# Kernel optimization log

Measured on AMD Instinct MI355X. Metric: run time of the kernel, lower is better.

## Reference

```python
import jax, jax.numpy as jnp
import numpy as np

N_NODES = 50000
N_EDGES = 800000
HIDDEN = 128
NUM_LAYERS = 3
NEG_SLOPE = 0.2  # PyG GATConv default leaky_relu slope


def setup_inputs() -> dict:
    key = jax.random.key(0)
    ks = jax.random.split(key, 10)
    d = HIDDEN
    glorot = 1.0 / np.sqrt(d)
    inp = {
        "x": jax.random.normal(ks[0], (N_NODES, d), dtype=jnp.float32),
        "edge_index": jax.random.randint(ks[1], (2, N_EDGES), 0, N_NODES, dtype=jnp.int32),
        "edge_mask": jax.random.uniform(ks[2], (N_EDGES,), dtype=jnp.float32),
        # GATConv params (heads=1)
        "W_gat": jax.random.normal(ks[3], (d, d), dtype=jnp.float32) * glorot,
        "a_src": jax.random.normal(ks[4], (d,), dtype=jnp.float32) * glorot,
        "a_dst": jax.random.normal(ks[5], (d,), dtype=jnp.float32) * glorot,
        "b_gat": jnp.zeros((d,), dtype=jnp.float32),
        # Stacked GCNConv params
        "W_gcn": jax.random.normal(ks[6], (NUM_LAYERS, d, d), dtype=jnp.float32) * glorot,
        "b_gcn": jnp.zeros((NUM_LAYERS, d), dtype=jnp.float32),
    }
    return inp


def _seg_softmax(e, seg, n):
    m = jax.ops.segment_max(e, seg, num_segments=n)
    p = jnp.exp(e - m[seg])
    s = jax.ops.segment_sum(p, seg, num_segments=n)
    return p / s[seg]


def reference(x, edge_index, edge_mask, W_gat, a_src, a_dst, b_gat, W_gcn, b_gcn):
    N = x.shape[0]
    loops = jnp.arange(N, dtype=edge_index.dtype)
    src = jnp.concatenate([edge_index[0], loops])  # [E+N] with self loops
    dst = jnp.concatenate([edge_index[1], loops])

    # --- GATConv (heads=1, add_self_loops=True); edge_attr ignored (edge_dim=None) ---
    xp = x @ W_gat                                      # [N, d]
    e = jax.nn.leaky_relu((xp @ a_src)[src] + (xp @ a_dst)[dst], NEG_SLOPE)
    alpha = _seg_softmax(e, dst, N)                     # segment softmax over incoming edges
    h = jax.ops.segment_sum(alpha[:, None] * xp[src], dst, num_segments=N) + b_gat

    # --- GCN normalization with edge_mask as edge_weight (self-loop weight = 1) ---
    w = jnp.concatenate([edge_mask, jnp.ones((N,), dtype=edge_mask.dtype)])
    deg = jax.ops.segment_sum(w, dst, num_segments=N)
    dinv = jnp.where(deg > 0, jax.lax.rsqrt(jnp.maximum(deg, 1e-12)), 0.0)
    norm = dinv[src] * w * dinv[dst]                    # [E+N]

    outs = [h]
    for l in range(NUM_LAYERS):
        z = outs[-1] @ W_gcn[l]                         # [N, d]
        z = jax.ops.segment_sum(norm[:, None] * z[src], dst, num_segments=N) + b_gcn[l]
        outs.append(jax.nn.relu(z))

    # JumpingKnowledge 'max': elementwise max over layer outputs
    return jnp.max(jnp.stack(outs, axis=0), axis=0)
```

## Files before the change

### kernel.cpp

```cpp
#include <hip/hip_runtime.h>

#define HIDDEN 128
#define NEG_SLOPE 0.2f
#define P_SORT 256

typedef unsigned short ushort_t;
typedef __attribute__((ext_vector_type(8))) short short8;
typedef __attribute__((ext_vector_type(4))) float floatx4;

static inline size_t align_up(size_t x, size_t a){ return (x + a - 1) & ~(a - 1); }

__device__ __forceinline__ ushort_t f2b(float f){
  unsigned u = __float_as_uint(f);
  unsigned r = (u + 0x7FFFu + ((u >> 16) & 1u)) >> 16;
  return (ushort_t)r;
}

__device__ __forceinline__ void fma8(float* acc, uint4 v, float a){
  acc[0] += a * __uint_as_float(v.x << 16);
  acc[1] += a * __uint_as_float(v.x & 0xFFFF0000u);
  acc[2] += a * __uint_as_float(v.y << 16);
  acc[3] += a * __uint_as_float(v.y & 0xFFFF0000u);
  acc[4] += a * __uint_as_float(v.z << 16);
  acc[5] += a * __uint_as_float(v.z & 0xFFFF0000u);
  acc[6] += a * __uint_as_float(v.w << 16);
  acc[7] += a * __uint_as_float(v.w & 0xFFFF0000u);
}

__device__ __forceinline__ uint4 pack8(const float* f){
  uint4 u;
  u.x = (unsigned)f2b(f[0]) | ((unsigned)f2b(f[1]) << 16);
  u.y = (unsigned)f2b(f[2]) | ((unsigned)f2b(f[3]) << 16);
  u.z = (unsigned)f2b(f[4]) | ((unsigned)f2b(f[5]) << 16);
  u.w = (unsigned)f2b(f[6]) | ((unsigned)f2b(f[7]) << 16);
  return u;
}


__global__ __launch_bounds__(256) void k_b1cnt(const int* __restrict__ dst,
                                               int* __restrict__ bcnt,
                                               int E, int epb, int nbkt){
  __shared__ unsigned c[256];
  int t = threadIdx.x;
  c[t] = 0;
  __syncthreads();
  int e0 = blockIdx.x * epb;
  int e1 = min(E, e0 + epb);
  for (int e = e0 + t; e < e1; e += 256) atomicAdd(&c[dst[e] >> 8], 1u);
  __syncthreads();
  if (t < nbkt) bcnt[t * P_SORT + blockIdx.x] = (int)c[t];
}

__global__ void k_scan1(const int* __restrict__ in, int* __restrict__ incl,
                        int* __restrict__ blockSums, int M){
  __shared__ int sd[256];
  int t = threadIdx.x;
  int i = blockIdx.x*256 + t;
  int v = (i < M) ? in[i] : 0;
  sd[t] = v; __syncthreads();
  for (int off = 1; off < 256; off <<= 1){
    int add = (t >= off) ? sd[t-off] : 0;
    __syncthreads();
    sd[t] += add;
    __syncthreads();
  }
  if (i < M) incl[i] = sd[t];
  if (t == 255) blockSums[blockIdx.x] = sd[255];
}

__global__ void k_scan2(const int* __restrict__ blockSums, int* __restrict__ blockOffs, int nb){
  __shared__ int sd[256];
  __shared__ int carry;
  int t = threadIdx.x;
  if (t == 0) carry = 0;
  __syncthreads();
  for (int base = 0; base < nb; base += 256){
    int i = base + t;
    int v = (i < nb) ? blockSums[i] : 0;
    sd[t] = v; __syncthreads();
    for (int off = 1; off < 256; off <<= 1){
      int add = (t >= off) ? sd[t-off] : 0;
      __syncthreads();
      sd[t] += add;
      __syncthreads();
    }
    if (i < nb) blockOffs[i] = carry + sd[t] - v;
    __syncthreads();
    if (t == 0) carry += sd[255];
    __syncthreads();
  }
}

__global__ void k_scanex(int* __restrict__ arr, const int* __restrict__ in,
                         const int* __restrict__ blockOffs, int M){
  int i = blockIdx.x*256 + threadIdx.x;
  if (i < M) arr[i] = arr[i] - in[i] + blockOffs[blockIdx.x];
}

__global__ __launch_bounds__(256) void k_b1place(const int* __restrict__ src,
                                                 const int* __restrict__ dst,
                                                 const float* __restrict__ w,
                                                 const int* __restrict__ ebase,
                                                 int2* __restrict__ tpw,
                                                 int E, int epb){
  __shared__ unsigned c[256];
  int t = threadIdx.x;
  c[t] = 0;
  __syncthreads();
  int e0 = blockIdx.x * epb;
  int e1 = min(E, e0 + epb);
  for (int e = e0 + t; e < e1; e += 256){
    int d = dst[e];
    int b = d >> 8;
    unsigned r = atomicAdd(&c[b], 1u);
    int pos = ebase[b * P_SORT + blockIdx.x] + (int)r;
    tpw[pos] = make_int2((int)((unsigned)src[e] | ((unsigned)(d & 255) << 16)),
                         __float_as_int(w[e]));
  }
}

__global__ __launch_bounds__(256) void k_b2(const int2* __restrict__ tpw,
                                            const int* __restrict__ ebase,
                                            int2* __restrict__ col_sw,
                                            int* __restrict__ rowp,
                                            float* __restrict__ dinv,
                                            int N, int E, int nbkt){
  __shared__ unsigned hcnt[256];
  __shared__ int sd[256];
  __shared__ int lofs[256];
  __shared__ unsigned rcnt[256];
  __shared__ float wsum[256];
  int b = blockIdx.x, t = threadIdx.x;
  int e0 = ebase[b * P_SORT];
  int e1 = (b + 1 < nbkt) ? ebase[(b + 1) * P_SORT] : E;
  hcnt[t] = 0; rcnt[t] = 0; wsum[t] = 0.f;
  __syncthreads();
  for (int e = e0 + t; e < e1; e += 256)
    atomicAdd(&hcnt[((unsigned)tpw[e].x >> 16) & 255u], 1u);
  __syncthreads();
  int v = (int)hcnt[t];
  sd[t] = v; __syncthreads();
  for (int off = 1; off < 256; off <<= 1){
    int add = (t >= off) ? sd[t-off] : 0;
    __syncthreads();
    sd[t] += add;
    __syncthreads();
  }
  lofs[t] = sd[t] - v;
  int node = b*256 + t;
  if (node < N) rowp[node] = e0 + sd[t] - v;
  if (b == 0 && t == 0) rowp[N] = E;
  __syncthreads();
  for (int e = e0 + t; e < e1; e += 256){
    int2 pw = tpw[e];
    unsigned dl = ((unsigned)pw.x >> 16) & 255u;
    unsigned r = atomicAdd(&rcnt[dl], 1u);
    int pos = e0 + lofs[dl] + (int)r;
    col_sw[pos] = make_int2((int)((unsigned)pw.x & 0xFFFFu), pw.y);
    atomicAdd(&wsum[dl], __int_as_float(pw.y));
  }
  __syncthreads();
  if (node < N) dinv[node] = rsqrtf(wsum[t] + 1.0f);
}


__global__ void k_cast_x(const float* __restrict__ x, unsigned* __restrict__ xb, long n2){
  long i = (long)blockIdx.x*256 + threadIdx.x;
  if (i >= n2) return;
  float2 v = ((const float2*)x)[i];
  xb[i] = (unsigned)f2b(v.x) | ((unsigned)f2b(v.y) << 16);
}

__global__ void k_cast_w(const float* __restrict__ Wg, const float* __restrict__ Wc,
                         ushort_t* __restrict__ Wt){
  int i = blockIdx.x*256 + threadIdx.x;
  int mat = i >> 14, idx = i & 16383;
  int k = idx >> 7, n = idx & 127;
  float v = (mat == 0) ? Wg[idx] : Wc[(mat-1)*16384 + idx];
  Wt[mat*16384 + n*128 + k] = f2b(v);
}

template<int DOTS>
__global__ __launch_bounds__(256) void k_gemm(const ushort_t* __restrict__ A,
                                              const ushort_t* __restrict__ Wt,
                                              ushort_t* __restrict__ C,
                                              const float* __restrict__ a_src,
                                              const float* __restrict__ a_dst,
                                              const float* __restrict__ dinv,
                                              float2* __restrict__ attr,
                                              float* __restrict__ sdst, int M){
  int wave = threadIdx.x >> 6, l = threadIdx.x & 63;
  int q = l >> 4, lm = l & 15;
  int rowBase = blockIdx.x*128 + wave*32;
  floatx4 acc[2][8];
  #pragma unroll
  for (int mt = 0; mt < 2; mt++)
    #pragma unroll
    for (int nt = 0; nt < 8; nt++) acc[mt][nt] = (floatx4){0.f,0.f,0.f,0.f};

  #pragma unroll
  for (int kc = 0; kc < 4; kc++){
    int k0 = kc*32 + q*8;
    short8 a[2];
    #pragma unroll
    for (int mt = 0; mt < 2; mt++){
      long r = rowBase + mt*16 + lm;
      if (r < M) a[mt] = *(const short8*)(A + r*128 + k0);
      else       a[mt] = (short8){0,0,0,0,0,0,0,0};
    }
    #pragma unroll
    for (int nt = 0; nt < 8; nt++){
      short8 b = *(const short8*)(Wt + (nt*16 + lm)*128 + k0);
      acc[0][nt] = __builtin_amdgcn_mfma_f32_16x16x32_bf16(a[0], b, acc[0][nt], 0, 0, 0);
      acc[1][nt] = __builtin_amdgcn_mfma_f32_16x16x32_bf16(a[1], b, acc[1][nt], 0, 0, 0);
    }
  }
  #pragma unroll
  for (int mt = 0; mt < 2; mt++){
    #pragma unroll
    for (int r = 0; r < 4; r++){
      long row = rowBase + mt*16 + q*4 + r;
      if (row < M){
        #pragma unroll
        for (int nt = 0; nt < 8; nt++)
          C[row*128 + nt*16 + lm] = f2b(acc[mt][nt][r]);
      }
    }
  }
  if (DOTS){
    float as8[8], ad8[8];
    #pragma unroll
    for (int nt = 0; nt < 8; nt++){ as8[nt] = a_src[nt*16 + lm]; ad8[nt] = a_dst[nt*16 + lm]; }
    #pragma unroll
    for (int mt = 0; mt < 2; mt++){
      #pragma unroll
      for (int r = 0; r < 4; r++){
        float ps = 0.f, pd = 0.f;
        #pragma unroll
        for (int nt = 0; nt < 8; nt++){
          ps += acc[mt][nt][r] * as8[nt];
          pd += acc[mt][nt][r] * ad8[nt];
        }
        #pragma unroll
        for (int off = 1; off <= 8; off <<= 1){
          ps += __shfl_xor(ps, off, 64);
          pd += __shfl_xor(pd, off, 64);
        }
        long row = rowBase + mt*16 + q*4 + r;
        if (lm == 0 && row < M){
          attr[row] = make_float2(ps, dinv[row]);
          sdst[row] = pd;
        }
      }
    }
  }
}

__global__ void k_post(const int* __restrict__ rowp, const int2* __restrict__ col_sw,
                       const float2* __restrict__ attr, const float* __restrict__ sdst,
                       int2* __restrict__ col_en, int2* __restrict__ col_ea,
                       float2* __restrict__ nparm, int N){
  int n = blockIdx.x*16 + (threadIdx.x >> 4);
  int l = threadIdx.x & 15;
  if (n >= N) return;
  int rs = rowp[n], re = rowp[n+1];
  float2 an = attr[n];
  float dn = an.y, sdd = sdst[n];
  float es = an.x + sdd;
  es = (es >= 0.f) ? es : NEG_SLOPE*es;
  float pself = __expf(es);
  float ps = 0.f;
  for (int j = rs + l; j < re; j += 16){
    int2 sw = col_sw[j];
    int s = sw.x;
    float w = __int_as_float(sw.y);
    float2 a = attr[s];
    col_en[j] = make_int2(s, __float_as_int(a.y * w * dn));
    float ee = a.x + sdd;
    ee = (ee >= 0.f) ? ee : NEG_SLOPE*ee;
    float pe = __expf(ee);
    ps += pe;
    col_ea[j] = make_int2(s, __float_as_int(pe));
  }
  ps += __shfl_xor(ps, 1); ps += __shfl_xor(ps, 2);
  ps += __shfl_xor(ps, 4); ps += __shfl_xor(ps, 8);
  if (l == 0){
    float inv = 1.f / (ps + pself);
    nparm[n] = make_float2(inv, pself * inv);
  }
}

template<int MODE>
__global__ __launch_bounds__(256) void k_agg(const ushort_t* __restrict__ feat,
                                             const int* __restrict__ rowp,
                                             const int2* __restrict__ col,
                                             const float2* __restrict__ np,
                                             const float* __restrict__ dinv,
                                             const float* __restrict__ bias,
                                             ushort_t* __restrict__ out, int N){
  int n = blockIdx.x*4 + (threadIdx.x >> 6);
  if (n >= N) return;
  int l = threadIdx.x & 63;
  int sub = l >> 4, q = l & 15;
  int rs = rowp[n], re = rowp[n+1];
  const uint4* f16 = (const uint4*)feat;
  float acc[8] = {0.f,0.f,0.f,0.f,0.f,0.f,0.f,0.f};
  for (int base = rs; base < re; base += 24){
    int2 p[6]; float a[6];
    #pragma unroll
    for (int j = 0; j < 6; j++){
      int e = base + sub + 4*j;
      int cc = min(e, re-1);
      p[j] = col[cc];
      a[j] = (e < re) ? __int_as_float(p[j].y) : 0.f;
    }
    uint4 v[6];
    #pragma unroll
    for (int j = 0; j < 6; j++) v[j] = f16[(size_t)p[j].x*16 + q];
    #pragma unroll
    for (int j = 0; j < 6; j++) fma8(acc, v[j], a[j]);
  }
  #pragma unroll
  for (int j = 0; j < 8; j++){
    acc[j] += __shfl_xor(acc[j], 16, 64);
    acc[j] += __shfl_xor(acc[j], 32, 64);
  }
  if (sub == 0){
    float sc;
    if (MODE == 0){
      float2 pp = np[n];
      #pragma unroll
      for (int j = 0; j < 8; j++) acc[j] *= pp.x;
      sc = pp.y;
    } else {
      float di = dinv[n];
      sc = di * di;
    }
    uint4 v = f16[(size_t)n*16 + q];
    fma8(acc, v, sc);
    float4 b0 = ((const float4*)bias)[q*2];
    float4 b1 = ((const float4*)bias)[q*2 + 1];
    acc[0]+=b0.x; acc[1]+=b0.y; acc[2]+=b0.z; acc[3]+=b0.w;
    acc[4]+=b1.x; acc[5]+=b1.y; acc[6]+=b1.z; acc[7]+=b1.w;
    if (MODE == 1){
      #pragma unroll
      for (int j = 0; j < 8; j++) acc[j] = fmaxf(acc[j], 0.f);
    }
    ((uint4*)out)[(size_t)n*16 + q] = pack8(acc);
  }
}

__global__ void k_jk(const uint4* __restrict__ h0, const uint4* __restrict__ h1,
                     const uint4* __restrict__ h2, const uint4* __restrict__ h3,
                     float4* __restrict__ out, long n16){
  long i = (long)blockIdx.x*256 + threadIdx.x;
  if (i >= n16) return;
  uint4 a = h0[i], b = h1[i], c = h2[i], d = h3[i];
  float m[8];
  #pragma unroll
  for (int j = 0; j < 4; j++){
    unsigned ua = (&a.x)[j], ub = (&b.x)[j], uc = (&c.x)[j], ud = (&d.x)[j];
    float lo = fmaxf(fmaxf(__uint_as_float(ua << 16), __uint_as_float(ub << 16)),
                     fmaxf(__uint_as_float(uc << 16), __uint_as_float(ud << 16)));
    float hi = fmaxf(fmaxf(__uint_as_float(ua & 0xFFFF0000u), __uint_as_float(ub & 0xFFFF0000u)),
                     fmaxf(__uint_as_float(uc & 0xFFFF0000u), __uint_as_float(ud & 0xFFFF0000u)));
    m[j*2] = lo; m[j*2+1] = hi;
  }
  out[i*2]   = make_float4(m[0], m[1], m[2], m[3]);
  out[i*2+1] = make_float4(m[4], m[5], m[6], m[7]);
}

extern "C" void kernel_launch(void* const* d_in, const int* in_sizes, int n_in,
                              void* d_out, int out_size, void* d_ws, size_t ws_size,
                              hipStream_t stream){
  const float* x      = (const float*)d_in[0];
  const int*   eidx   = (const int*)d_in[1];
  const float* emask  = (const float*)d_in[2];
  const float* W_gat  = (const float*)d_in[3];
  const float* a_src  = (const float*)d_in[4];
  const float* a_dst  = (const float*)d_in[5];
  const float* b_gat  = (const float*)d_in[6];
  const float* W_gcn  = (const float*)d_in[7];
  const float* b_gcn  = (const float*)d_in[8];
  int N = in_sizes[0] / HIDDEN;
  int E = in_sizes[1] / 2;
  const int* src = eidx;
  const int* dst = eidx + E;

  char* p = (char*)d_ws;
  auto carve = [&](size_t bytes)->char*{ char* q = p; p += align_up(bytes, 512); return q; };
  ushort_t* xb   = (ushort_t*)carve((size_t)N*HIDDEN*2);
  ushort_t* zb   = (ushort_t*)carve((size_t)N*HIDDEN*2);
  ushort_t* h0   = (ushort_t*)carve((size_t)N*HIDDEN*2);
  ushort_t* h1   = (ushort_t*)carve((size_t)N*HIDDEN*2);
  ushort_t* h2   = (ushort_t*)carve((size_t)N*HIDDEN*2);
  ushort_t* h3   = (ushort_t*)carve((size_t)N*HIDDEN*2);
  ushort_t* Wt   = (ushort_t*)carve((size_t)4*HIDDEN*HIDDEN*2);
  float2* attr   = (float2*)carve((size_t)N*8);
  float2* nparm  = (float2*)carve((size_t)N*8);
  float* sdst    = (float*)carve((size_t)N*4);
  float* dinv    = (float*)carve((size_t)N*4);
  int*   rowp    = (int*)  carve((size_t)(N+1)*4);
  int2*  col_sw  = (int2*) carve((size_t)E*8);
  int2*  col_en  = (int2*) carve((size_t)E*8);
  int2*  col_ea  = (int2*) carve((size_t)E*8);
  int2*  tpw     = (int2*) carve((size_t)E*8);
  int nbkt = (N + 255) >> 8;
  int M    = nbkt * P_SORT;
  int*   bcnt  = (int*)carve((size_t)M*4);
  int*   ebase = (int*)carve((size_t)M*4);
  int nbs = (M + 255) / 256;
  int*   blockSums = (int*)carve((size_t)nbs*4);
  int*   blockOffs = (int*)carve((size_t)nbs*4);
  (void)ws_size; (void)n_in; (void)out_size;

  int epb = (E + P_SORT - 1) / P_SORT;
  int gb  = (N + 127) / 128;
  int nwb = (N + 3) / 4;
  int nqb = (N + 15) / 16;
  long n2 = (long)N*64;
  int cb  = (int)((n2 + 255) / 256);
  long n16 = (long)N*16;
  int jb  = (int)((n16 + 255) / 256);

  k_b1cnt  <<<P_SORT, 256, 0, stream>>>(dst, bcnt, E, epb, nbkt);
  k_scan1  <<<nbs, 256, 0, stream>>>(bcnt, ebase, blockSums, M);
  k_scan2  <<<1,   256, 0, stream>>>(blockSums, blockOffs, nbs);
  k_scanex <<<nbs, 256, 0, stream>>>(ebase, bcnt, blockOffs, M);
  k_b1place<<<P_SORT, 256, 0, stream>>>(src, dst, emask, ebase, tpw, E, epb);
  k_b2     <<<nbkt, 256, 0, stream>>>(tpw, ebase, col_sw, rowp, dinv, N, E, nbkt);

  k_cast_x<<<cb, 256, 0, stream>>>(x, (unsigned*)xb, n2);
  k_cast_w<<<(4*HIDDEN*HIDDEN)/256, 256, 0, stream>>>(W_gat, W_gcn, Wt);

  k_gemm<1><<<gb, 256, 0, stream>>>(xb, Wt, zb, a_src, a_dst, dinv, attr, sdst, N);
  k_post<<<nqb, 256, 0, stream>>>(rowp, col_sw, attr, sdst, col_en, col_ea, nparm, N);

  k_agg<0><<<nwb, 256, 0, stream>>>(zb, rowp, col_ea, nparm, dinv, b_gat, h0, N);
  ushort_t* hs[4] = {h0, h1, h2, h3};
  for (int l = 0; l < 3; l++){
    k_gemm<0><<<gb, 256, 0, stream>>>(hs[l], Wt + (size_t)(l+1)*HIDDEN*HIDDEN, zb,
                                      a_src, a_dst, dinv, attr, sdst, N);
    k_agg<1><<<nwb, 256, 0, stream>>>(zb, rowp, col_en, nparm, dinv,
                                      b_gcn + (size_t)l*HIDDEN, hs[l+1], N);
  }
  k_jk<<<jb, 256, 0, stream>>>((const uint4*)h0, (const uint4*)h1,
                               (const uint4*)h2, (const uint4*)h3,
                               (float4*)d_out, n16);
}
```

Baseline: 350.5 us.

## Fuse scan fixup, x cast, attention post-pass and JK max into neighbors

Removes four kernels by folding their work into adjacent ones. The exclusive-scan fixup moves into the placement kernel, which computes bucket bases in shared memory. The fp32-to-bf16 cast of x moves into the first GEMM's load path. The attention softmax post-pass (edge exp and per-node normalizer) moves into the GAT aggregation kernel, and the jumping-knowledge max moves into the last GCN aggregation's epilogue. The aim is to cut launch count and intermediate global-memory round trips. In exchange, the fused GAT aggregation computes softmax terms with a less parallel per-wave loop before it aggregates.

```diff
diff --git a/kernel.cpp b/kernel.cpp
--- a/kernel.cpp
+++ b/kernel.cpp
@@ -91,21 +91,22 @@
   }
 }
 
-__global__ void k_scanex(int* __restrict__ arr, const int* __restrict__ in,
-                         const int* __restrict__ blockOffs, int M){
-  int i = blockIdx.x*256 + threadIdx.x;
-  if (i < M) arr[i] = arr[i] - in[i] + blockOffs[blockIdx.x];
-}
-
 __global__ __launch_bounds__(256) void k_b1place(const int* __restrict__ src,
                                                  const int* __restrict__ dst,
                                                  const float* __restrict__ w,
-                                                 const int* __restrict__ ebase,
+                                                 const int* __restrict__ incl,
+                                                 const int* __restrict__ bcnt,
+                                                 const int* __restrict__ blockOffs,
                                                  int2* __restrict__ tpw,
-                                                 int E, int epb){
+                                                 int E, int epb, int nbkt){
+  __shared__ int base_[256];
   __shared__ unsigned c[256];
   int t = threadIdx.x;
   c[t] = 0;
+  if (t < nbkt){
+    int idx = t * P_SORT + blockIdx.x;
+    base_[t] = incl[idx] - bcnt[idx] + blockOffs[t];
+  }
   __syncthreads();
   int e0 = blockIdx.x * epb;
   int e1 = min(E, e0 + epb);
@@ -113,14 +114,14 @@
     int d = dst[e];
     int b = d >> 8;
     unsigned r = atomicAdd(&c[b], 1u);
-    int pos = ebase[b * P_SORT + blockIdx.x] + (int)r;
+    int pos = base_[b] + (int)r;
     tpw[pos] = make_int2((int)((unsigned)src[e] | ((unsigned)(d & 255) << 16)),
                          __float_as_int(w[e]));
   }
 }
 
 __global__ __launch_bounds__(256) void k_b2(const int2* __restrict__ tpw,
-                                            const int* __restrict__ ebase,
+                                            const int* __restrict__ blockOffs,
                                             int2* __restrict__ col_sw,
                                             int* __restrict__ rowp,
                                             float* __restrict__ dinv,
@@ -131,8 +132,8 @@
   __shared__ unsigned rcnt[256];
   __shared__ float wsum[256];
   int b = blockIdx.x, t = threadIdx.x;
-  int e0 = ebase[b * P_SORT];
-  int e1 = (b + 1 < nbkt) ? ebase[(b + 1) * P_SORT] : E;
+  int e0 = blockOffs[b];
+  int e1 = (b + 1 < nbkt) ? blockOffs[b + 1] : E;
   hcnt[t] = 0; rcnt[t] = 0; wsum[t] = 0.f;
   __syncthreads();
   for (int e = e0 + t; e < e1; e += 256)
@@ -164,13 +165,6 @@
 }
 
 
-__global__ void k_cast_x(const float* __restrict__ x, unsigned* __restrict__ xb, long n2){
-  long i = (long)blockIdx.x*256 + threadIdx.x;
-  if (i >= n2) return;
-  float2 v = ((const float2*)x)[i];
-  xb[i] = (unsigned)f2b(v.x) | ((unsigned)f2b(v.y) << 16);
-}
-
 __global__ void k_cast_w(const float* __restrict__ Wg, const float* __restrict__ Wc,
                          ushort_t* __restrict__ Wt){
   int i = blockIdx.x*256 + threadIdx.x;
@@ -181,7 +175,7 @@
 }
 
 template<int DOTS>
-__global__ __launch_bounds__(256) void k_gemm(const ushort_t* __restrict__ A,
+__global__ __launch_bounds__(256) void k_gemm(const void* __restrict__ Ain,
                                               const ushort_t* __restrict__ Wt,
                                               ushort_t* __restrict__ C,
                                               const float* __restrict__ a_src,
@@ -205,8 +199,19 @@
     #pragma unroll
     for (int mt = 0; mt < 2; mt++){
       long r = rowBase + mt*16 + lm;
-      if (r < M) a[mt] = *(const short8*)(A + r*128 + k0);
-      else       a[mt] = (short8){0,0,0,0,0,0,0,0};
+      if (r < M){
+        if (DOTS){
+          const float* ap = (const float*)Ain + r*128 + k0;
+          float4 u = *(const float4*)ap;
+          float4 v = *(const float4*)(ap + 4);
+          short8 tv;
+          tv[0]=(short)f2b(u.x); tv[1]=(short)f2b(u.y); tv[2]=(short)f2b(u.z); tv[3]=(short)f2b(u.w);
+          tv[4]=(short)f2b(v.x); tv[5]=(short)f2b(v.y); tv[6]=(short)f2b(v.z); tv[7]=(short)f2b(v.w);
+          a[mt] = tv;
+        } else {
+          a[mt] = *(const short8*)((const ushort_t*)Ain + r*128 + k0);
+        }
+      } else a[mt] = (short8){0,0,0,0,0,0,0,0};
     }
     #pragma unroll
     for (int nt = 0; nt < 8; nt++){
@@ -256,53 +261,50 @@
   }
 }
 
-__global__ void k_post(const int* __restrict__ rowp, const int2* __restrict__ col_sw,
-                       const float2* __restrict__ attr, const float* __restrict__ sdst,
-                       int2* __restrict__ col_en, int2* __restrict__ col_ea,
-                       float2* __restrict__ nparm, int N){
-  int n = blockIdx.x*16 + (threadIdx.x >> 4);
-  int l = threadIdx.x & 15;
-  if (n >= N) return;
-  int rs = rowp[n], re = rowp[n+1];
-  float2 an = attr[n];
-  float dn = an.y, sdd = sdst[n];
-  float es = an.x + sdd;
-  es = (es >= 0.f) ? es : NEG_SLOPE*es;
-  float pself = __expf(es);
-  float ps = 0.f;
-  for (int j = rs + l; j < re; j += 16){
-    int2 sw = col_sw[j];
-    int s = sw.x;
-    float w = __int_as_float(sw.y);
-    float2 a = attr[s];
-    col_en[j] = make_int2(s, __float_as_int(a.y * w * dn));
-    float ee = a.x + sdd;
-    ee = (ee >= 0.f) ? ee : NEG_SLOPE*ee;
-    float pe = __expf(ee);
-    ps += pe;
-    col_ea[j] = make_int2(s, __float_as_int(pe));
-  }
-  ps += __shfl_xor(ps, 1); ps += __shfl_xor(ps, 2);
-  ps += __shfl_xor(ps, 4); ps += __shfl_xor(ps, 8);
-  if (l == 0){
-    float inv = 1.f / (ps + pself);
-    nparm[n] = make_float2(inv, pself * inv);
-  }
-}
-
 template<int MODE>
 __global__ __launch_bounds__(256) void k_agg(const ushort_t* __restrict__ feat,
                                              const int* __restrict__ rowp,
-                                             const int2* __restrict__ col,
-                                             const float2* __restrict__ np,
+                                             const int2* __restrict__ col_sw,
+                                             int2* __restrict__ col_en,
+                                             int2* __restrict__ col_ea,
+                                             const float2* __restrict__ attr,
+                                             const float* __restrict__ sdst_,
                                              const float* __restrict__ dinv,
                                              const float* __restrict__ bias,
-                                             ushort_t* __restrict__ out, int N){
+                                             ushort_t* __restrict__ out,
+                                             const uint4* __restrict__ j0,
+                                             const uint4* __restrict__ j1,
+                                             const uint4* __restrict__ j2,
+                                             float4* __restrict__ yout, int N){
   int n = blockIdx.x*4 + (threadIdx.x >> 6);
   if (n >= N) return;
   int l = threadIdx.x & 63;
+  int rs = rowp[n], re = rowp[n+1];
+  float inv = 0.f, pself = 0.f;
+  if (MODE == 0){
+    float2 an = attr[n];
+    float sdd = sdst_[n];
+    float es = an.x + sdd;
+    es = (es >= 0.f) ? es : NEG_SLOPE*es;
+    pself = __expf(es);
+    float ps = 0.f;
+    for (int j = rs + l; j < re; j += 64){
+      int2 sw = col_sw[j];
+      float w = __int_as_float(sw.y);
+      float2 a = attr[sw.x];
+      col_en[j] = make_int2(sw.x, __float_as_int(a.y * w * an.y));
+      float ee = a.x + sdd;
+      ee = (ee >= 0.f) ? ee : NEG_SLOPE*ee;
+      float pe = __expf(ee);
+      ps += pe;
+      col_ea[j] = make_int2(sw.x, __float_as_int(pe));
+    }
+    #pragma unroll
+    for (int off = 32; off >= 1; off >>= 1) ps += __shfl_xor(ps, off, 64);
+    inv = 1.f / (ps + pself);
+  }
+  const int2* col = (MODE == 0) ? (const int2*)col_ea : (const int2*)col_en;
   int sub = l >> 4, q = l & 15;
-  int rs = rowp[n], re = rowp[n+1];
   const uint4* f16 = (const uint4*)feat;
   float acc[8] = {0.f,0.f,0.f,0.f,0.f,0.f,0.f,0.f};
   for (int base = rs; base < re; base += 24){
@@ -328,10 +330,9 @@
   if (sub == 0){
     float sc;
     if (MODE == 0){
-      float2 pp = np[n];
       #pragma unroll
-      for (int j = 0; j < 8; j++) acc[j] *= pp.x;
-      sc = pp.y;
+      for (int j = 0; j < 8; j++) acc[j] *= inv;
+      sc = pself * inv;
     } else {
       float di = dinv[n];
       sc = di * di;
@@ -342,32 +343,31 @@
     float4 b1 = ((const float4*)bias)[q*2 + 1];
     acc[0]+=b0.x; acc[1]+=b0.y; acc[2]+=b0.z; acc[3]+=b0.w;
     acc[4]+=b1.x; acc[5]+=b1.y; acc[6]+=b1.z; acc[7]+=b1.w;
-    if (MODE == 1){
+    if (MODE >= 1){
       #pragma unroll
       for (int j = 0; j < 8; j++) acc[j] = fmaxf(acc[j], 0.f);
     }
-    ((uint4*)out)[(size_t)n*16 + q] = pack8(acc);
-  }
-}
-
-__global__ void k_jk(const uint4* __restrict__ h0, const uint4* __restrict__ h1,
-                     const uint4* __restrict__ h2, const uint4* __restrict__ h3,
-                     float4* __restrict__ out, long n16){
-  long i = (long)blockIdx.x*256 + threadIdx.x;
-  if (i >= n16) return;
-  uint4 a = h0[i], b = h1[i], c = h2[i], d = h3[i];
-  float m[8];
-  #pragma unroll
-  for (int j = 0; j < 4; j++){
-    unsigned ua = (&a.x)[j], ub = (&b.x)[j], uc = (&c.x)[j], ud = (&d.x)[j];
-    float lo = fmaxf(fmaxf(__uint_as_float(ua << 16), __uint_as_float(ub << 16)),
-                     fmaxf(__uint_as_float(uc << 16), __uint_as_float(ud << 16)));
-    float hi = fmaxf(fmaxf(__uint_as_float(ua & 0xFFFF0000u), __uint_as_float(ub & 0xFFFF0000u)),
-                     fmaxf(__uint_as_float(uc & 0xFFFF0000u), __uint_as_float(ud & 0xFFFF0000u)));
-    m[j*2] = lo; m[j*2+1] = hi;
-  }
-  out[i*2]   = make_float4(m[0], m[1], m[2], m[3]);
-  out[i*2+1] = make_float4(m[4], m[5], m[6], m[7]);
+    if (MODE <= 1){
+      ((uint4*)out)[(size_t)n*16 + q] = pack8(acc);
+    } else {
+      size_t qi = (size_t)n*16 + q;
+      uint4 a0 = j0[qi], a1 = j1[qi], a2 = j2[qi];
+      float m[8];
+      #pragma unroll
+      for (int k = 0; k < 4; k++){
+        unsigned u0 = (&a0.x)[k], u1 = (&a1.x)[k], u2 = (&a2.x)[k];
+        float lo = fmaxf(fmaxf(__uint_as_float(u0 << 16), __uint_as_float(u1 << 16)),
+                         __uint_as_float(u2 << 16));
+        float hi = fmaxf(fmaxf(__uint_as_float(u0 & 0xFFFF0000u), __uint_as_float(u1 & 0xFFFF0000u)),
+                         __uint_as_float(u2 & 0xFFFF0000u));
+        m[k*2]   = fmaxf(acc[k*2],   lo);
+        m[k*2+1] = fmaxf(acc[k*2+1], hi);
+      }
+      size_t yi = (size_t)n*32 + q*2;
+      yout[yi]   = make_float4(m[0], m[1], m[2], m[3]);
+      yout[yi+1] = make_float4(m[4], m[5], m[6], m[7]);
+    }
+  }
 }
 
 extern "C" void kernel_launch(void* const* d_in, const int* in_sizes, int n_in,
@@ -389,15 +389,12 @@
 
   char* p = (char*)d_ws;
   auto carve = [&](size_t bytes)->char*{ char* q = p; p += align_up(bytes, 512); return q; };
-  ushort_t* xb   = (ushort_t*)carve((size_t)N*HIDDEN*2);
   ushort_t* zb   = (ushort_t*)carve((size_t)N*HIDDEN*2);
   ushort_t* h0   = (ushort_t*)carve((size_t)N*HIDDEN*2);
   ushort_t* h1   = (ushort_t*)carve((size_t)N*HIDDEN*2);
   ushort_t* h2   = (ushort_t*)carve((size_t)N*HIDDEN*2);
-  ushort_t* h3   = (ushort_t*)carve((size_t)N*HIDDEN*2);
   ushort_t* Wt   = (ushort_t*)carve((size_t)4*HIDDEN*HIDDEN*2);
   float2* attr   = (float2*)carve((size_t)N*8);
-  float2* nparm  = (float2*)carve((size_t)N*8);
   float* sdst    = (float*)carve((size_t)N*4);
   float* dinv    = (float*)carve((size_t)N*4);
   int*   rowp    = (int*)  carve((size_t)(N+1)*4);
@@ -408,7 +405,7 @@
   int nbkt = (N + 255) >> 8;
   int M    = nbkt * P_SORT;
   int*   bcnt  = (int*)carve((size_t)M*4);
-  int*   ebase = (int*)carve((size_t)M*4);
+  int*   incl  = (int*)carve((size_t)M*4);
   int nbs = (M + 255) / 256;
   int*   blockSums = (int*)carve((size_t)nbs*4);
   int*   blockOffs = (int*)carve((size_t)nbs*4);
@@ -417,34 +414,33 @@
   int epb = (E + P_SORT - 1) / P_SORT;
   int gb  = (N + 127) / 128;
   int nwb = (N + 3) / 4;
-  int nqb = (N + 15) / 16;
-  long n2 = (long)N*64;
-  int cb  = (int)((n2 + 255) / 256);
-  long n16 = (long)N*16;
-  int jb  = (int)((n16 + 255) / 256);
 
   k_b1cnt  <<<P_SORT, 256, 0, stream>>>(dst, bcnt, E, epb, nbkt);
-  k_scan1  <<<nbs, 256, 0, stream>>>(bcnt, ebase, blockSums, M);
+  k_scan1  <<<nbs, 256, 0, stream>>>(bcnt, incl, blockSums, M);
   k_scan2  <<<1,   256, 0, stream>>>(blockSums, blockOffs, nbs);
-  k_scanex <<<nbs, 256, 0, stream>>>(ebase, bcnt, blockOffs, M);
-  k_b1place<<<P_SORT, 256, 0, stream>>>(src, dst, emask, ebase, tpw, E, epb);
-  k_b2     <<<nbkt, 256, 0, stream>>>(tpw, ebase, col_sw, rowp, dinv, N, E, nbkt);
-
-  k_cast_x<<<cb, 256, 0, stream>>>(x, (unsigned*)xb, n2);
+  k_b1place<<<P_SORT, 256, 0, stream>>>(src, dst, emask, incl, bcnt, blockOffs,
+                                        tpw, E, epb, nbkt);
+  k_b2     <<<nbkt, 256, 0, stream>>>(tpw, blockOffs, col_sw, rowp, dinv, N, E, nbkt);
+
   k_cast_w<<<(4*HIDDEN*HIDDEN)/256, 256, 0, stream>>>(W_gat, W_gcn, Wt);
 
-  k_gemm<1><<<gb, 256, 0, stream>>>(xb, Wt, zb, a_src, a_dst, dinv, attr, sdst, N);
-  k_post<<<nqb, 256, 0, stream>>>(rowp, col_sw, attr, sdst, col_en, col_ea, nparm, N);
-
-  k_agg<0><<<nwb, 256, 0, stream>>>(zb, rowp, col_ea, nparm, dinv, b_gat, h0, N);
-  ushort_t* hs[4] = {h0, h1, h2, h3};
-  for (int l = 0; l < 3; l++){
-    k_gemm<0><<<gb, 256, 0, stream>>>(hs[l], Wt + (size_t)(l+1)*HIDDEN*HIDDEN, zb,
-                                      a_src, a_dst, dinv, attr, sdst, N);
-    k_agg<1><<<nwb, 256, 0, stream>>>(zb, rowp, col_en, nparm, dinv,
-                                      b_gcn + (size_t)l*HIDDEN, hs[l+1], N);
-  }
-  k_jk<<<jb, 256, 0, stream>>>((const uint4*)h0, (const uint4*)h1,
-                               (const uint4*)h2, (const uint4*)h3,
-                               (float4*)d_out, n16);
-}
+  k_gemm<1><<<gb, 256, 0, stream>>>((const void*)x, Wt, zb, a_src, a_dst, dinv, attr, sdst, N);
+
+  k_agg<0><<<nwb, 256, 0, stream>>>(zb, rowp, col_sw, col_en, col_ea, attr, sdst,
+                                    dinv, b_gat, h0, nullptr, nullptr, nullptr, nullptr, N);
+
+  ushort_t* hs[3] = {h0, h1, h2};
+  for (int l = 0; l < 2; l++){
+    k_gemm<0><<<gb, 256, 0, stream>>>((const void*)hs[l], Wt + (size_t)(l+1)*HIDDEN*HIDDEN,
+                                      zb, a_src, a_dst, dinv, attr, sdst, N);
+    k_agg<1><<<nwb, 256, 0, stream>>>(zb, rowp, col_sw, col_en, col_ea, attr, sdst,
+                                      dinv, b_gcn + (size_t)l*HIDDEN, hs[l+1],
+                                      nullptr, nullptr, nullptr, nullptr, N);
+  }
+  k_gemm<0><<<gb, 256, 0, stream>>>((const void*)h2, Wt + (size_t)3*HIDDEN*HIDDEN,
+                                    zb, a_src, a_dst, dinv, attr, sdst, N);
+  k_agg<2><<<nwb, 256, 0, stream>>>(zb, rowp, col_sw, col_en, col_ea, attr, sdst,
+                                    dinv, b_gcn + (size_t)2*HIDDEN, nullptr,
+                                    (const uint4*)h0, (const uint4*)h1, (const uint4*)h2,
+                                    (float4*)d_out, N);
+}
```

Result: faster. 342.7 us (-2.2%).
